# Kernel tuning notes

Hardware: AMD Instinct MI355X
Metric: run time of the kernel (lower is better)

Reference implementation:

```python
import jax, jax.numpy as jnp
import numpy as np
import math

D = 128  # hidden_dim
N_USERS = 10000
N_ITEMS = 12000
NEG_INF = -9e15


def setup_inputs() -> dict:
    key = jax.random.key(0)
    k1, k2, k3, k4, k5 = jax.random.split(key, 5)
    ufea = jax.random.normal(k1, (N_USERS, D), dtype=jnp.float32)
    inter = jax.random.normal(k2, (N_ITEMS, D), dtype=jnp.float32)
    adj = jax.random.randint(k3, (N_USERS, N_ITEMS), 0, 2, dtype=jnp.int32)
    # linear layer params (torch default init approximated with scaled normals)
    W = jax.random.normal(k4, (D, D), dtype=jnp.float32) / jnp.sqrt(jnp.float32(D))
    b = jax.random.normal(k5, (D,), dtype=jnp.float32) * 0.01
    return {"ufea": ufea, "inter": inter, "adj": adj, "W": W, "b": b}


def _leaky_relu2(x):
    # nn.LeakyReLU(2): negative_slope = 2
    return jnp.where(x > 0, x, 2.0 * x)


def reference(ufea, inter, adj, W, b):
    # GAT.forward_user with dropout in eval mode (identity).
    # Attention.forward(a=ufea, b=inter, adj)
    query = ufea @ W.T + b                      # [N, D]  nn.Linear
    scale = 1.0 / math.sqrt(D)
    scores = _leaky_relu2((query @ inter.T) * scale)   # [N, M]
    scores = jnp.where(adj > 0, scores, NEG_INF)        # mask non-edges
    attn = jax.nn.softmax(scores, axis=1)               # row softmax
    result = attn @ inter                                # [N, D]
    return result
```

## Files before the change

### kernel.cpp

```cpp
#include <hip/hip_runtime.h>
#include <cstdint>
#include <cstddef>


#define N_USERS 10000
#define N_ITEMS 12000
#define HD      128
#define QROWS   10112
#define NCHUNK  12
#define TILE    64
#define NTILES  188
#define UBLOCKS 79
#define QBLOCKS 632

typedef __bf16 bf16x8 __attribute__((ext_vector_type(8)));
typedef __bf16 bf16x4 __attribute__((ext_vector_type(4)));
typedef float  f32x4  __attribute__((ext_vector_type(4)));
typedef int    i32x4  __attribute__((ext_vector_type(4)));

typedef const __attribute__((address_space(1))) unsigned int g_u32;
typedef __attribute__((address_space(3))) unsigned int l_u32;

__global__ __launch_bounds__(256) void prep_kernel(const float* __restrict__ inter,
                                                   const float* __restrict__ ufea,
                                                   const float* __restrict__ W,
                                                   const float* __restrict__ bias,
                                                   __bf16* __restrict__ kvg,
                                                   __bf16* __restrict__ qg) {
    __shared__ __bf16 Tl[128 * 72];
    const int t = threadIdx.x;
    const int lane = t & 63, wave = t >> 6;
    const int n = lane & 15, qd = lane >> 4;

    if (blockIdx.x < NTILES) {
        const int tile = blockIdx.x;
        const int i0 = tile * 64;
        for (int it = 0; it < 8; ++it) {
            int g   = it * 256 + t;
            int row = g >> 5;
            int d   = (g & 31) * 4;
            int item = i0 + row;
            if (item < N_ITEMS) {
                f32x4 v = *(const f32x4*)(inter + (size_t)item * HD + d);
                Tl[(d + 0) * 72 + row] = (__bf16)v.x;
                Tl[(d + 1) * 72 + row] = (__bf16)v.y;
                Tl[(d + 2) * 72 + row] = (__bf16)v.z;
                Tl[(d + 3) * 72 + row] = (__bf16)v.w;
            } else {
                Tl[(d + 0) * 72 + row] = (__bf16)0.f;
                Tl[(d + 1) * 72 + row] = (__bf16)0.f;
                Tl[(d + 2) * 72 + row] = (__bf16)0.f;
                Tl[(d + 3) * 72 + row] = (__bf16)0.f;
            }
        }
        __syncthreads();
        __bf16* tbase = kvg + (size_t)tile * (32 * 512);
        #pragma unroll
        for (int j = 0; j < 4; ++j) {
            const int c = wave * 4 + j;
            int row = i0 + 4 * n + wave;
            bf16x8 o;
            if (row < N_ITEMS) {
                const float* p = inter + (size_t)row * HD + j * 32 + qd * 8;
                f32x4 lo = *(const f32x4*)p, hi = *(const f32x4*)(p + 4);
                o[0]=(__bf16)lo.x; o[1]=(__bf16)lo.y; o[2]=(__bf16)lo.z; o[3]=(__bf16)lo.w;
                o[4]=(__bf16)hi.x; o[5]=(__bf16)hi.y; o[6]=(__bf16)hi.z; o[7]=(__bf16)hi.w;
            } else {
                #pragma unroll
                for (int e = 0; e < 8; ++e) o[e] = (__bf16)0.f;
            }
            *(bf16x8*)(tbase + (size_t)c * 512 + lane * 8) = o;
        }
        #pragma unroll
        for (int j = 0; j < 4; ++j) {
            const int cc = wave * 4 + j;
            const int dt = cc >> 1, kc = cc & 1;
            bf16x8 v = *(const bf16x8*)&Tl[(dt * 16 + n) * 72 + kc * 32 + qd * 8];
            *(bf16x8*)(tbase + (size_t)(16 + cc) * 512 + lane * 8) = v;
        }
    } else {
        const int user0 = (blockIdx.x - NTILES) * 16;
        int arow = user0 + n; if (arow > N_USERS - 1) arow = N_USERS - 1;

        bf16x8 af[4];
        #pragma unroll
        for (int kk = 0; kk < 4; ++kk) {
            const float* p = ufea + (size_t)arow * HD + kk * 32 + qd * 8;
            f32x4 lo = *(const f32x4*)p, hi = *(const f32x4*)(p + 4);
            bf16x8 a;
            a[0]=(__bf16)lo.x; a[1]=(__bf16)lo.y; a[2]=(__bf16)lo.z; a[3]=(__bf16)lo.w;
            a[4]=(__bf16)hi.x; a[5]=(__bf16)hi.y; a[6]=(__bf16)hi.z; a[7]=(__bf16)hi.w;
            af[kk] = a;
        }
        #pragma unroll
        for (int h = 0; h < 2; ++h) {
            const int nt = wave * 2 + h;
            f32x4 acc = {0.f, 0.f, 0.f, 0.f};
            #pragma unroll
            for (int kk = 0; kk < 4; ++kk) {
                const float* p = W + (size_t)(nt * 16 + n) * HD + kk * 32 + qd * 8;
                f32x4 lo = *(const f32x4*)p, hi = *(const f32x4*)(p + 4);
                bf16x8 b;
                b[0]=(__bf16)lo.x; b[1]=(__bf16)lo.y; b[2]=(__bf16)lo.z; b[3]=(__bf16)lo.w;
                b[4]=(__bf16)hi.x; b[5]=(__bf16)hi.y; b[6]=(__bf16)hi.z; b[7]=(__bf16)hi.w;
                acc = __builtin_amdgcn_mfma_f32_16x16x32_bf16(af[kk], b, acc, 0, 0, 0);
            }
            const float bv = bias[nt * 16 + n];
            #pragma unroll
            for (int r = 0; r < 4; ++r) {
                int row = user0 + qd * 4 + r;
                qg[(size_t)row * HD + nt * 16 + n] = (__bf16)(acc[r] + bv);
            }
        }
    }
}

__global__ __launch_bounds__(256, 2) void fused_kernel(const __bf16* __restrict__ qg,
                                                       const __bf16* __restrict__ kvg,
                                                       const int* __restrict__ adj,
                                                       float* __restrict__ Opart,
                                                       float* __restrict__ lpart) {
    __shared__ __bf16 Kbuf[2][16 * 512];
    __shared__ __bf16 Vbuf[16 * 512];
    __shared__ __bf16 Pl[4][32 * 72];
    const int lane = threadIdx.x & 63, wave = threadIdx.x >> 6;
    const int n = lane & 15, qd = lane >> 4;
    const int user0 = blockIdx.y * 128 + wave * 32;
    const int chunk = blockIdx.x;
    const int t0 = (chunk * NTILES) / NCHUNK;
    const int t1 = ((chunk + 1) * NTILES) / NCHUNK;
    const float SC = (float)(1.4426950408889634 * 0.08838834764831845);

    bf16x8 qf[2][4];
    #pragma unroll
    for (int g = 0; g < 2; ++g)
        #pragma unroll
        for (int kk = 0; kk < 4; ++kk)
            qf[g][kk] = *(const bf16x8*)(qg + (size_t)(user0 + g * 16 + n) * HD + kk * 32 + qd * 8);

    f32x4 Oacc[2][8];
    #pragma unroll
    for (int g = 0; g < 2; ++g)
        #pragma unroll
        for (int dt = 0; dt < 8; ++dt) Oacc[g][dt] = (f32x4){0.f, 0.f, 0.f, 0.f};
    float lacc[2][4] = {{0.f,0.f,0.f,0.f},{0.f,0.f,0.f,0.f}};

    int adjOff[2][4];
    #pragma unroll
    for (int g = 0; g < 2; ++g)
        #pragma unroll
        for (int r = 0; r < 4; ++r) {
            int u = user0 + g * 16 + qd * 4 + r;
            if (u > N_USERS - 1) u = N_USERS - 1;
            adjOff[g][r] = u * N_ITEMS;
        }
    __bf16* pw = &Pl[wave][0];

    i32x4 avA[2][4], avB[2][4];
    {
        const __bf16* tb = kvg + (size_t)t0 * (32 * 512);
        #pragma unroll
        for (int j = 0; j < 4; ++j) {
            const int c = wave * 4 + j;
            __builtin_amdgcn_global_load_lds((g_u32*)(tb + (size_t)c * 512 + lane * 8),
                                             (l_u32*)(&Kbuf[0][c * 512]), 16, 0, 0);
        }
        #pragma unroll
        for (int j = 0; j < 4; ++j) {
            const int c = wave * 4 + j;
            __builtin_amdgcn_global_load_lds((g_u32*)(tb + (size_t)(16 + c) * 512 + lane * 8),
                                             (l_u32*)(&Vbuf[c * 512]), 16, 0, 0);
        }
        int col4 = t0 * TILE + 4 * n;
        if (col4 > N_ITEMS - 4) col4 = N_ITEMS - 4;
        #pragma unroll
        for (int g = 0; g < 2; ++g)
            #pragma unroll
            for (int r = 0; r < 4; ++r)
                avA[g][r] = __builtin_nontemporal_load((const i32x4*)(adj + adjOff[g][r] + col4));
    }
    __syncthreads();

    auto tile_iter = [&](int T, int cur, i32x4 (&avu)[2][4], i32x4 (&avp)[2][4]) {
        const int j0 = T * TILE;
        const bool more = (T + 1 < t1);
        const __bf16* tbn = kvg + (size_t)(T + 1) * (32 * 512);

        if (more) {
            #pragma unroll
            for (int j = 0; j < 4; ++j) {
                const int c = wave * 4 + j;
                __builtin_amdgcn_global_load_lds((g_u32*)(tbn + (size_t)c * 512 + lane * 8),
                                                 (l_u32*)(&Kbuf[cur ^ 1][c * 512]), 16, 0, 0);
            }
        }
        {
            int tn = T + 1; if (tn > t1 - 1) tn = t1 - 1;
            int col4 = tn * TILE + 4 * n;
            if (col4 > N_ITEMS - 4) col4 = N_ITEMS - 4;
            #pragma unroll
            for (int g = 0; g < 2; ++g)
                #pragma unroll
                for (int r = 0; r < 4; ++r)
                    avp[g][r] = __builtin_nontemporal_load((const i32x4*)(adj + adjOff[g][r] + col4));
        }

        f32x4 S[2][4];
        #pragma unroll
        for (int g = 0; g < 2; ++g)
            #pragma unroll
            for (int nt = 0; nt < 4; ++nt) S[g][nt] = (f32x4){0.f, 0.f, 0.f, 0.f};
        const __bf16* kb = &Kbuf[cur][0];
        #pragma unroll
        for (int nt = 0; nt < 4; ++nt) {
            #pragma unroll
            for (int kk = 0; kk < 4; ++kk) {
                bf16x8 b = *(const bf16x8*)(kb + (nt * 4 + kk) * 512 + lane * 8);
                S[0][nt] = __builtin_amdgcn_mfma_f32_16x16x32_bf16(qf[0][kk], b, S[0][nt], 0, 0, 0);
                S[1][nt] = __builtin_amdgcn_mfma_f32_16x16x32_bf16(qf[1][kk], b, S[1][nt], 0, 0, 0);
            }
        }

        #pragma unroll
        for (int g = 0; g < 2; ++g) {
            #pragma unroll
            for (int r = 0; r < 4; ++r) {
                bf16x4 pk;
                #pragma unroll
                for (int nt = 0; nt < 4; ++nt) {
                    float s = S[g][nt][r] * SC;
                    s = fminf(s, s + s);
                    const bool on = (j0 + 4 * n + nt < N_ITEMS) && (avu[g][r][nt] > 0);
                    float p = on ? __builtin_amdgcn_exp2f(s) : 0.f;
                    lacc[g][r] += p;
                    pk[nt] = (__bf16)p;
                }
                *(bf16x4*)(pw + (g * 16 + qd * 4 + r) * 72 + 4 * n) = pk;
            }
        }

        __syncthreads();

        #pragma unroll
        for (int kc = 0; kc < 2; ++kc) {
            bf16x8 af0 = *(const bf16x8*)(pw + (0 * 16 + n) * 72 + kc * 32 + qd * 8);
            bf16x8 af1 = *(const bf16x8*)(pw + (1 * 16 + n) * 72 + kc * 32 + qd * 8);
            #pragma unroll
            for (int dt = 0; dt < 8; ++dt) {
                bf16x8 b = *(const bf16x8*)(&Vbuf[(dt * 2 + kc) * 512 + lane * 8]);
                Oacc[0][dt] = __builtin_amdgcn_mfma_f32_16x16x32_bf16(af0, b, Oacc[0][dt], 0, 0, 0);
                Oacc[1][dt] = __builtin_amdgcn_mfma_f32_16x16x32_bf16(af1, b, Oacc[1][dt], 0, 0, 0);
            }
        }

        __syncthreads();

        if (more) {
            #pragma unroll
            for (int j = 0; j < 4; ++j) {
                const int c = wave * 4 + j;
                __builtin_amdgcn_global_load_lds((g_u32*)(tbn + (size_t)(16 + c) * 512 + lane * 8),
                                                 (l_u32*)(&Vbuf[c * 512]), 16, 0, 0);
            }
        }
    };

    int T = t0;
    while (true) {
        tile_iter(T, 0, avA, avB); ++T; if (T >= t1) break;
        tile_iter(T, 1, avB, avA); ++T; if (T >= t1) break;
    }

    #pragma unroll
    for (int g = 0; g < 2; ++g)
        #pragma unroll
        for (int r = 0; r < 4; ++r) {
            float v = lacc[g][r];
            v += __shfl_xor(v, 1);
            v += __shfl_xor(v, 2);
            v += __shfl_xor(v, 4);
            v += __shfl_xor(v, 8);
            lacc[g][r] = v;
        }
    const size_t cb = (size_t)chunk * QROWS;
    #pragma unroll
    for (int g = 0; g < 2; ++g)
        #pragma unroll
        for (int r = 0; r < 4; ++r) {
            const int user = user0 + g * 16 + qd * 4 + r;
            if (user < N_USERS) {
                #pragma unroll
                for (int dt = 0; dt < 8; ++dt)
                    Opart[(cb + user) * HD + dt * 16 + n] = Oacc[g][dt][r];
                if (n == 0) lpart[cb + user] = lacc[g][r];
            }
        }
}

__global__ __launch_bounds__(256) void combine_kernel(const float* __restrict__ Opart,
                                                      const float* __restrict__ lpart,
                                                      float* __restrict__ out) {
    const int g = blockIdx.x * 256 + threadIdx.x;
    const int base = g * 4;
    const int user = base >> 7;
    const int d = base & 127;
    f32x4 acc = {0.f, 0.f, 0.f, 0.f};
    float l = 0.f;
    #pragma unroll
    for (int c = 0; c < NCHUNK; ++c) {
        acc += *(const f32x4*)(Opart + ((size_t)c * QROWS + user) * HD + d);
        l += lpart[(size_t)c * QROWS + user];
    }
    if (user < N_USERS) {
        f32x4 res = acc / l;
        *(f32x4*)(out + (size_t)user * HD + d) = res;
    }
}

extern "C" void kernel_launch(void* const* d_in, const int* in_sizes, int n_in,
                              void* d_out, int out_size, void* d_ws, size_t ws_size,
                              hipStream_t stream) {
    const float* ufea = (const float*)d_in[0];
    const float* inter = (const float*)d_in[1];
    const int*   adj  = (const int*)d_in[2];
    const float* W    = (const float*)d_in[3];
    const float* bias = (const float*)d_in[4];
    float* out = (float*)d_out;

    char* ws = (char*)d_ws;
    __bf16* kvg  = (__bf16*)(ws);
    __bf16* qg   = (__bf16*)(ws + 6160384);
    float*  Opart = (float*)(ws + 8749056);
    float*  lpart = (float*)(ws + 70877184);

    prep_kernel<<<dim3(NTILES + QBLOCKS), dim3(256), 0, stream>>>(inter, ufea, W, bias, kvg, qg);
    fused_kernel<<<dim3(NCHUNK, UBLOCKS), dim3(256), 0, stream>>>(qg, kvg, adj, Opart, lpart);
    combine_kernel<<<dim3(1264), dim3(256), 0, stream>>>(Opart, lpart, out);
}
```

Before: 663.9 us.

## Drop K/adj double-buffering to fit three blocks per CU

Replaces the double-buffered K tile and the register-prefetched adjacency tile with a single-buffered per-tile load followed by a barrier. This frees enough LDS and registers to raise the occupancy target from 2 to 3 blocks per CU. Adjacency values are packed into bitmasks to cut register use, and the out-of-range column check now runs only on the last partial tile. The cost is losing the software overlap of global loads with compute, so latency hiding now depends on more resident waves.

Result: slower. 936.2 us (+41.0%).

```diff
diff --git a/kernel.cpp b/kernel.cpp
--- a/kernel.cpp
+++ b/kernel.cpp
@@ -115,12 +115,12 @@
     }
 }
 
-__global__ __launch_bounds__(256, 2) void fused_kernel(const __bf16* __restrict__ qg,
+__global__ __launch_bounds__(256, 3) void fused_kernel(const __bf16* __restrict__ qg,
                                                        const __bf16* __restrict__ kvg,
                                                        const int* __restrict__ adj,
                                                        float* __restrict__ Opart,
                                                        float* __restrict__ lpart) {
-    __shared__ __bf16 Kbuf[2][16 * 512];
+    __shared__ __bf16 Kbuf[16 * 512];
     __shared__ __bf16 Vbuf[16 * 512];
     __shared__ __bf16 Pl[4][32 * 72];
     const int lane = threadIdx.x & 63, wave = threadIdx.x >> 6;
@@ -156,14 +156,17 @@
         }
     __bf16* pw = &Pl[wave][0];
 
-    i32x4 avA[2][4], avB[2][4];
-    {
-        const __bf16* tb = kvg + (size_t)t0 * (32 * 512);
+    for (int T = t0; T < t1; ++T) {
+        const int j0 = T * TILE;
+        const __bf16* tb = kvg + (size_t)T * (32 * 512);
+
+        __builtin_amdgcn_s_barrier();
+
         #pragma unroll
         for (int j = 0; j < 4; ++j) {
             const int c = wave * 4 + j;
             __builtin_amdgcn_global_load_lds((g_u32*)(tb + (size_t)c * 512 + lane * 8),
-                                             (l_u32*)(&Kbuf[0][c * 512]), 16, 0, 0);
+                                             (l_u32*)(&Kbuf[c * 512]), 16, 0, 0);
         }
         #pragma unroll
         for (int j = 0; j < 4; ++j) {
@@ -171,75 +174,64 @@
             __builtin_amdgcn_global_load_lds((g_u32*)(tb + (size_t)(16 + c) * 512 + lane * 8),
                                              (l_u32*)(&Vbuf[c * 512]), 16, 0, 0);
         }
-        int col4 = t0 * TILE + 4 * n;
-        if (col4 > N_ITEMS - 4) col4 = N_ITEMS - 4;
-        #pragma unroll
-        for (int g = 0; g < 2; ++g)
-            #pragma unroll
-            for (int r = 0; r < 4; ++r)
-                avA[g][r] = __builtin_nontemporal_load((const i32x4*)(adj + adjOff[g][r] + col4));
-    }
-    __syncthreads();
-
-    auto tile_iter = [&](int T, int cur, i32x4 (&avu)[2][4], i32x4 (&avp)[2][4]) {
-        const int j0 = T * TILE;
-        const bool more = (T + 1 < t1);
-        const __bf16* tbn = kvg + (size_t)(T + 1) * (32 * 512);
-
-        if (more) {
-            #pragma unroll
-            for (int j = 0; j < 4; ++j) {
-                const int c = wave * 4 + j;
-                __builtin_amdgcn_global_load_lds((g_u32*)(tbn + (size_t)c * 512 + lane * 8),
-                                                 (l_u32*)(&Kbuf[cur ^ 1][c * 512]), 16, 0, 0);
-            }
-        }
+        i32x4 av[2][4];
         {
-            int tn = T + 1; if (tn > t1 - 1) tn = t1 - 1;
-            int col4 = tn * TILE + 4 * n;
+            int col4 = j0 + 4 * n;
             if (col4 > N_ITEMS - 4) col4 = N_ITEMS - 4;
             #pragma unroll
             for (int g = 0; g < 2; ++g)
                 #pragma unroll
                 for (int r = 0; r < 4; ++r)
-                    avp[g][r] = __builtin_nontemporal_load((const i32x4*)(adj + adjOff[g][r] + col4));
-        }
+                    av[g][r] = __builtin_nontemporal_load((const i32x4*)(adj + adjOff[g][r] + col4));
+        }
+        __syncthreads();
+
+        unsigned m0 = 0, m1 = 0;
+        #pragma unroll
+        for (int r = 0; r < 4; ++r)
+            #pragma unroll
+            for (int nt = 0; nt < 4; ++nt) {
+                m0 |= (unsigned)(av[0][r][nt] & 1) << (r * 4 + nt);
+                m1 |= (unsigned)(av[1][r][nt] & 1) << (r * 4 + nt);
+            }
 
         f32x4 S[2][4];
         #pragma unroll
         for (int g = 0; g < 2; ++g)
             #pragma unroll
             for (int nt = 0; nt < 4; ++nt) S[g][nt] = (f32x4){0.f, 0.f, 0.f, 0.f};
-        const __bf16* kb = &Kbuf[cur][0];
         #pragma unroll
         for (int nt = 0; nt < 4; ++nt) {
             #pragma unroll
             for (int kk = 0; kk < 4; ++kk) {
-                bf16x8 b = *(const bf16x8*)(kb + (nt * 4 + kk) * 512 + lane * 8);
+                bf16x8 b = *(const bf16x8*)(&Kbuf[(nt * 4 + kk) * 512 + lane * 8]);
                 S[0][nt] = __builtin_amdgcn_mfma_f32_16x16x32_bf16(qf[0][kk], b, S[0][nt], 0, 0, 0);
                 S[1][nt] = __builtin_amdgcn_mfma_f32_16x16x32_bf16(qf[1][kk], b, S[1][nt], 0, 0, 0);
             }
         }
 
-        #pragma unroll
-        for (int g = 0; g < 2; ++g) {
-            #pragma unroll
-            for (int r = 0; r < 4; ++r) {
-                bf16x4 pk;
+        auto mask_body = [&](bool EDGE) {
+            #pragma unroll
+            for (int g = 0; g < 2; ++g) {
+                const unsigned mg = g ? m1 : m0;
                 #pragma unroll
-                for (int nt = 0; nt < 4; ++nt) {
-                    float s = S[g][nt][r] * SC;
-                    s = fminf(s, s + s);
-                    const bool on = (j0 + 4 * n + nt < N_ITEMS) && (avu[g][r][nt] > 0);
-                    float p = on ? __builtin_amdgcn_exp2f(s) : 0.f;
-                    lacc[g][r] += p;
-                    pk[nt] = (__bf16)p;
+                for (int r = 0; r < 4; ++r) {
+                    bf16x4 pk;
+                    #pragma unroll
+                    for (int nt = 0; nt < 4; ++nt) {
+                        float s = S[g][nt][r] * SC;
+                        s = fminf(s, s + s);
+                        bool on = (mg >> (r * 4 + nt)) & 1;
+                        if (EDGE) on = on && (j0 + 4 * n + nt < N_ITEMS);
+                        float p = on ? __builtin_amdgcn_exp2f(s) : 0.f;
+                        lacc[g][r] += p;
+                        pk[nt] = (__bf16)p;
+                    }
+                    *(bf16x4*)(pw + (g * 16 + qd * 4 + r) * 72 + 4 * n) = pk;
                 }
-                *(bf16x4*)(pw + (g * 16 + qd * 4 + r) * 72 + 4 * n) = pk;
-            }
-        }
-
-        __syncthreads();
+            }
+        };
+        if (j0 + TILE > N_ITEMS) mask_body(true); else mask_body(false);
 
         #pragma unroll
         for (int kc = 0; kc < 2; ++kc) {
@@ -252,23 +244,6 @@
                 Oacc[1][dt] = __builtin_amdgcn_mfma_f32_16x16x32_bf16(af1, b, Oacc[1][dt], 0, 0, 0);
             }
         }
-
-        __syncthreads();
-
-        if (more) {
-            #pragma unroll
-            for (int j = 0; j < 4; ++j) {
-                const int c = wave * 4 + j;
-                __builtin_amdgcn_global_load_lds((g_u32*)(tbn + (size_t)(16 + c) * 512 + lane * 8),
-                                                 (l_u32*)(&Vbuf[c * 512]), 16, 0, 0);
-            }
-        }
-    };
-
-    int T = t0;
-    while (true) {
-        tile_iter(T, 0, avA, avB); ++T; if (T >= t1) break;
-        tile_iter(T, 1, avB, avA); ++T; if (T >= t1) break;
     }
 
     #pragma unroll
```

## Pack adjacency into per-tile bitmasks in prep kernel and halve item chunks

Applied to the files above, without the earlier changes.

Adds blocks to the prep kernel that compress each user's 64-item adjacency tile into a 64-bit mask. The fused attention kernel then reads one u64 per row per tile instead of 64 int32 values, which removes most adjacency traffic from the hot loop and the register double-buffering that went with it. The item-chunk count drops from 12 to 6, shrinking the partial-output buffers and combine work but giving the fused kernel fewer blocks. The full int32 adjacency is still read once in prep, so the saving depends on overlap and on the smaller fused-kernel footprint.

Measured after the change: 730.7 us. 1.1x slower.

```diff
diff --git a/kernel.cpp b/kernel.cpp
--- a/kernel.cpp
+++ b/kernel.cpp
@@ -7,16 +7,19 @@
 #define N_ITEMS 12000
 #define HD      128
 #define QROWS   10112
-#define NCHUNK  12
+#define NCHUNK  6
 #define TILE    64
 #define NTILES  188
 #define UBLOCKS 79
 #define QBLOCKS 632
+#define AMBLOCKS 1228
+#define NWORDS  (N_USERS * NTILES)
 
 typedef __bf16 bf16x8 __attribute__((ext_vector_type(8)));
 typedef __bf16 bf16x4 __attribute__((ext_vector_type(4)));
 typedef float  f32x4  __attribute__((ext_vector_type(4)));
 typedef int    i32x4  __attribute__((ext_vector_type(4)));
+typedef unsigned long long u64;
 
 typedef const __attribute__((address_space(1))) unsigned int g_u32;
 typedef __attribute__((address_space(3))) unsigned int l_u32;
@@ -25,8 +28,10 @@
                                                    const float* __restrict__ ufea,
                                                    const float* __restrict__ W,
                                                    const float* __restrict__ bias,
+                                                   const int* __restrict__ adj,
                                                    __bf16* __restrict__ kvg,
-                                                   __bf16* __restrict__ qg) {
+                                                   __bf16* __restrict__ qg,
+                                                   u64* __restrict__ mask) {
     __shared__ __bf16 Tl[128 * 72];
     const int t = threadIdx.x;
     const int lane = t & 63, wave = t >> 6;
@@ -78,7 +83,7 @@
             bf16x8 v = *(const bf16x8*)&Tl[(dt * 16 + n) * 72 + kc * 32 + qd * 8];
             *(bf16x8*)(tbase + (size_t)(16 + cc) * 512 + lane * 8) = v;
         }
-    } else {
+    } else if (blockIdx.x < NTILES + QBLOCKS) {
         const int user0 = (blockIdx.x - NTILES) * 16;
         int arow = user0 + n; if (arow > N_USERS - 1) arow = N_USERS - 1;
 
@@ -112,12 +117,34 @@
                 qg[(size_t)row * HD + nt * 16 + n] = (__bf16)(acc[r] + bv);
             }
         }
+    } else {
+        const int gid = (blockIdx.x - (NTILES + QBLOCKS)) * 16 + (t >> 4);
+        for (int w = gid; w < NWORDS; w += AMBLOCKS * 16) {
+            const int u = w / NTILES;
+            const int T = w - u * NTILES;
+            const int col4 = T * 64 + 4 * n;
+            const int col4c = (col4 <= N_ITEMS - 4) ? col4 : (N_ITEMS - 16);
+            i32x4 av = __builtin_nontemporal_load(
+                (const i32x4*)(adj + (size_t)u * N_ITEMS + col4c));
+            unsigned nib = 0;
+            #pragma unroll
+            for (int nt = 0; nt < 4; ++nt)
+                if ((col4 + nt < N_ITEMS) && (av[nt] > 0)) nib |= 1u << nt;
+            unsigned lo = (n < 8) ? (nib << (4 * n)) : 0u;
+            unsigned hi = (n >= 8) ? (nib << (4 * (n - 8))) : 0u;
+            #pragma unroll
+            for (int m = 1; m < 16; m <<= 1) {
+                lo |= __shfl_xor(lo, m);
+                hi |= __shfl_xor(hi, m);
+            }
+            if (n == 0) mask[w] = ((u64)hi << 32) | lo;
+        }
     }
 }
 
 __global__ __launch_bounds__(256, 2) void fused_kernel(const __bf16* __restrict__ qg,
                                                        const __bf16* __restrict__ kvg,
-                                                       const int* __restrict__ adj,
+                                                       const u64* __restrict__ mask,
                                                        float* __restrict__ Opart,
                                                        float* __restrict__ lpart) {
     __shared__ __bf16 Kbuf[2][16 * 512];
@@ -145,18 +172,17 @@
         for (int dt = 0; dt < 8; ++dt) Oacc[g][dt] = (f32x4){0.f, 0.f, 0.f, 0.f};
     float lacc[2][4] = {{0.f,0.f,0.f,0.f},{0.f,0.f,0.f,0.f}};
 
-    int adjOff[2][4];
+    int maskRow[2][4];
     #pragma unroll
     for (int g = 0; g < 2; ++g)
         #pragma unroll
         for (int r = 0; r < 4; ++r) {
             int u = user0 + g * 16 + qd * 4 + r;
             if (u > N_USERS - 1) u = N_USERS - 1;
-            adjOff[g][r] = u * N_ITEMS;
+            maskRow[g][r] = u * NTILES;
         }
     __bf16* pw = &Pl[wave][0];
 
-    i32x4 avA[2][4], avB[2][4];
     {
         const __bf16* tb = kvg + (size_t)t0 * (32 * 512);
         #pragma unroll
@@ -171,18 +197,11 @@
             __builtin_amdgcn_global_load_lds((g_u32*)(tb + (size_t)(16 + c) * 512 + lane * 8),
                                              (l_u32*)(&Vbuf[c * 512]), 16, 0, 0);
         }
-        int col4 = t0 * TILE + 4 * n;
-        if (col4 > N_ITEMS - 4) col4 = N_ITEMS - 4;
-        #pragma unroll
-        for (int g = 0; g < 2; ++g)
-            #pragma unroll
-            for (int r = 0; r < 4; ++r)
-                avA[g][r] = __builtin_nontemporal_load((const i32x4*)(adj + adjOff[g][r] + col4));
     }
     __syncthreads();
 
-    auto tile_iter = [&](int T, int cur, i32x4 (&avu)[2][4], i32x4 (&avp)[2][4]) {
-        const int j0 = T * TILE;
+    int cur = 0;
+    for (int T = t0; T < t1; ++T) {
         const bool more = (T + 1 < t1);
         const __bf16* tbn = kvg + (size_t)(T + 1) * (32 * 512);
 
@@ -194,16 +213,12 @@
                                                  (l_u32*)(&Kbuf[cur ^ 1][c * 512]), 16, 0, 0);
             }
         }
-        {
-            int tn = T + 1; if (tn > t1 - 1) tn = t1 - 1;
-            int col4 = tn * TILE + 4 * n;
-            if (col4 > N_ITEMS - 4) col4 = N_ITEMS - 4;
-            #pragma unroll
-            for (int g = 0; g < 2; ++g)
-                #pragma unroll
-                for (int r = 0; r < 4; ++r)
-                    avp[g][r] = __builtin_nontemporal_load((const i32x4*)(adj + adjOff[g][r] + col4));
-        }
+        u64 mw[2][4];
+        #pragma unroll
+        for (int g = 0; g < 2; ++g)
+            #pragma unroll
+            for (int r = 0; r < 4; ++r)
+                mw[g][r] = mask[maskRow[g][r] + T];
 
         f32x4 S[2][4];
         #pragma unroll
@@ -225,12 +240,13 @@
         for (int g = 0; g < 2; ++g) {
             #pragma unroll
             for (int r = 0; r < 4; ++r) {
+                const unsigned nib = (unsigned)(mw[g][r] >> (4 * n)) & 0xFu;
                 bf16x4 pk;
                 #pragma unroll
                 for (int nt = 0; nt < 4; ++nt) {
                     float s = S[g][nt][r] * SC;
                     s = fminf(s, s + s);
-                    const bool on = (j0 + 4 * n + nt < N_ITEMS) && (avu[g][r][nt] > 0);
+                    const bool on = (nib >> nt) & 1u;
                     float p = on ? __builtin_amdgcn_exp2f(s) : 0.f;
                     lacc[g][r] += p;
                     pk[nt] = (__bf16)p;
@@ -263,12 +279,7 @@
                                                  (l_u32*)(&Vbuf[c * 512]), 16, 0, 0);
             }
         }
-    };
-
-    int T = t0;
-    while (true) {
-        tile_iter(T, 0, avA, avB); ++T; if (T >= t1) break;
-        tile_iter(T, 1, avB, avA); ++T; if (T >= t1) break;
+        cur ^= 1;
     }
 
     #pragma unroll
@@ -330,10 +341,12 @@
     char* ws = (char*)d_ws;
     __bf16* kvg  = (__bf16*)(ws);
     __bf16* qg   = (__bf16*)(ws + 6160384);
-    float*  Opart = (float*)(ws + 8749056);
-    float*  lpart = (float*)(ws + 70877184);
-
-    prep_kernel<<<dim3(NTILES + QBLOCKS), dim3(256), 0, stream>>>(inter, ufea, W, bias, kvg, qg);
-    fused_kernel<<<dim3(NCHUNK, UBLOCKS), dim3(256), 0, stream>>>(qg, kvg, adj, Opart, lpart);
+    u64*    mask = (u64*)(ws + 8749056);
+    float*  Opart = (float*)(ws + 23789056);
+    float*  lpart = (float*)(ws + 54853120);
+
+    prep_kernel<<<dim3(NTILES + QBLOCKS + AMBLOCKS), dim3(256), 0, stream>>>(
+        inter, ufea, W, bias, adj, kvg, qg, mask);
+    fused_kernel<<<dim3(NCHUNK, UBLOCKS), dim3(256), 0, stream>>>(qg, kvg, mask, Opart, lpart);
     combine_kernel<<<dim3(1264), dim3(256), 0, stream>>>(Opart, lpart, out);
 }
```
